# Kernel optimization log

Measured on AMD Instinct MI355X. Metric: run time of the kernel, lower is better.

## Reference

```python
import jax, jax.numpy as jnp
import numpy as np

N_NODES = 100000
N_EDGES = 1200000
IN_DIM, HID_DIM, OUT_DIM = 64, 64, 32


def setup_inputs() -> dict:
    key = jax.random.key(0)
    k1, k2, k3, k4, k5, k6 = jax.random.split(key, 6)
    x = jax.random.normal(k1, (N_NODES, IN_DIM), dtype=jnp.float32)
    edge_index = jax.random.randint(k2, (2, N_EDGES), 0, N_NODES, dtype=jnp.int64)
    # Glorot-style init for GCN linear weights
    W1 = jax.random.normal(k3, (IN_DIM, HID_DIM), dtype=jnp.float32) / np.sqrt(IN_DIM)
    b1 = jnp.zeros((HID_DIM,), dtype=jnp.float32)
    W2 = jax.random.normal(k4, (HID_DIM, OUT_DIM), dtype=jnp.float32) / np.sqrt(HID_DIM)
    b2 = jnp.zeros((OUT_DIM,), dtype=jnp.float32)
    return {"x": x, "edge_index": edge_index, "W1": W1, "b1": b1, "W2": W2, "b2": b2}


def _gcn_conv(x, W, b, src, dst, norm, n_nodes):
    # linear transform first (PyG GCNConv): [N, out]
    h = x @ W
    # gather messages along edges (incl. self-loops), scale by sym norm
    msg = h[src] * norm[:, None]            # [E+N, out]
    out = jax.ops.segment_sum(msg, dst, num_segments=n_nodes)
    return out + b


def reference(x, edge_index, W1, b1, W2, b2):
    n_nodes = x.shape[0]
    # add self-loops (PyG GCNConv default)
    loop = jnp.arange(n_nodes, dtype=edge_index.dtype)
    src = jnp.concatenate([edge_index[0], loop])
    dst = jnp.concatenate([edge_index[1], loop])
    # symmetric normalization: deg^{-1/2}[src] * deg^{-1/2}[dst]
    deg = jax.ops.segment_sum(jnp.ones_like(dst, dtype=x.dtype), dst, num_segments=n_nodes)
    deg_isqrt = jax.lax.rsqrt(deg)          # deg >= 1 due to self-loops
    norm = deg_isqrt[src] * deg_isqrt[dst]
    h = _gcn_conv(x, W1, b1, src, dst, norm, n_nodes)
    h = jax.nn.relu(h)
    out = _gcn_conv(h, W2, b2, src, dst, norm, n_nodes)
    return out
```

## Files before the change

### kernel.cpp

```cpp
#include <hip/hip_runtime.h>
#include <hip/hip_fp16.h>
#include <type_traits>

#define NBUCK 512
#define CH    2048

typedef _Float16 half8 __attribute__((ext_vector_type(8)));
typedef float floatx4 __attribute__((ext_vector_type(4)));

__device__ inline void unpack8(const float4& raw, float* f) {
    const __half2* p = (const __half2*)&raw;
#pragma unroll
    for (int i = 0; i < 4; ++i) {
        float2 t = __half22float2(p[i]);
        f[2 * i] = t.x;
        f[2 * i + 1] = t.y;
    }
}


__device__ inline void gemm64_f32_body(const float* __restrict__ X, const float* __restrict__ W,
                                       __half* __restrict__ H, int M, int ntiles, int vblk,
                                       int GB) {
    constexpr int NC = 4;
    const int lane = threadIdx.x & 63;
    const int wid  = threadIdx.x >> 6;
    const int q    = lane >> 4;
    const int m    = lane & 15;

    half8 bfrag[2][NC];
#pragma unroll
    for (int s = 0; s < 2; ++s)
#pragma unroll
        for (int c = 0; c < NC; ++c)
#pragma unroll
            for (int j = 0; j < 8; ++j)
                bfrag[s][c][j] = (_Float16)W[(s * 32 + q * 8 + j) * 64 + c * 16 + m];

    for (int tile = vblk * 4 + wid; tile < ntiles; tile += GB * 4) {
        int rowBase = tile * 16;
        int rowA = rowBase + m;
        if (rowA > M - 1) rowA = M - 1;

        half8 afrag[2];
        const float4* Xr = (const float4*)(X + (size_t)rowA * 64);
#pragma unroll
        for (int s = 0; s < 2; ++s) {
            float4 v0 = Xr[s * 8 + q * 2 + 0];
            float4 v1 = Xr[s * 8 + q * 2 + 1];
            afrag[s][0] = (_Float16)v0.x;
            afrag[s][1] = (_Float16)v0.y;
            afrag[s][2] = (_Float16)v0.z;
            afrag[s][3] = (_Float16)v0.w;
            afrag[s][4] = (_Float16)v1.x;
            afrag[s][5] = (_Float16)v1.y;
            afrag[s][6] = (_Float16)v1.z;
            afrag[s][7] = (_Float16)v1.w;
        }

        floatx4 acc[NC];
#pragma unroll
        for (int c = 0; c < NC; ++c) acc[c] = (floatx4){0.f, 0.f, 0.f, 0.f};
#pragma unroll
        for (int s = 0; s < 2; ++s)
#pragma unroll
            for (int c = 0; c < NC; ++c)
                acc[c] = __builtin_amdgcn_mfma_f32_16x16x32_f16(afrag[s], bfrag[s][c], acc[c],
                                                                0, 0, 0);

#pragma unroll
        for (int r = 0; r < 4; ++r) {
            int row = rowBase + q * 4 + r;
            if (row < M) {
#pragma unroll
                for (int c = 0; c < NC; ++c)
                    H[(size_t)row * 64 + c * 16 + m] = __float2half(acc[c][r]);
            }
        }
    }
}


__global__ __launch_bounds__(256) void hist_gemm1_kernel(
    const int* __restrict__ dst, int* __restrict__ blockHist,
    const float* __restrict__ X, const float* __restrict__ W1, __half* __restrict__ H,
    int M, int ntiles, int E, int R, int HB, int GB) {
    int blk = blockIdx.x;
    if (blk < HB) {
        __shared__ int h[NBUCK];
        int tid = threadIdx.x;
        for (int i = tid; i < NBUCK; i += 256) h[i] = 0;
        __syncthreads();
        int start = blk * CH;
        int count = E - start;
        if (count > CH) count = CH;
        for (int i = tid; i < count; i += 256) atomicAdd(&h[dst[start + i] / R], 1);
        __syncthreads();
        for (int i = tid; i < NBUCK; i += 256) blockHist[(size_t)blk * NBUCK + i] = h[i];
    } else {
        gemm64_f32_body(X, W1, H, M, ntiles, blk - HB, GB);
    }
}


__global__ __launch_bounds__(NBUCK) void scan_bases_kernel(const int* __restrict__ blockHist,
                                                           int* __restrict__ baseTbl,
                                                           int* __restrict__ bucketStart, int HB) {
    __shared__ int lds[NBUCK];
    int b = threadIdx.x;
    int running = 0;
    int k = 0;
    for (; k + 8 <= HB; k += 8) {
        int v[8];
#pragma unroll
        for (int u = 0; u < 8; ++u) v[u] = blockHist[(size_t)(k + u) * NBUCK + b];
#pragma unroll
        for (int u = 0; u < 8; ++u) {
            baseTbl[(size_t)(k + u) * NBUCK + b] = running;
            running += v[u];
        }
    }
    for (; k < HB; ++k) {
        int v = blockHist[(size_t)k * NBUCK + b];
        baseTbl[(size_t)k * NBUCK + b] = running;
        running += v;
    }
    lds[b] = running;
    __syncthreads();
    for (int off = 1; off < NBUCK; off <<= 1) {
        int x = (b >= off) ? lds[b - off] : 0;
        __syncthreads();
        lds[b] += x;
        __syncthreads();
    }
    bucketStart[b] = lds[b] - running;
    if (b == NBUCK - 1) bucketStart[NBUCK] = lds[b];
}


__global__ __launch_bounds__(256) void scatter_kernel(
    const int* __restrict__ src, const int* __restrict__ dst, const int* __restrict__ baseTbl,
    const int* __restrict__ bucketStart, unsigned long long* __restrict__ pairs, int E, int R) {
    __shared__ int lcur[NBUCK];
    int blk = blockIdx.x, tid = threadIdx.x;
    for (int i = tid; i < NBUCK; i += 256)
        lcur[i] = bucketStart[i] + baseTbl[(size_t)blk * NBUCK + i];
    __syncthreads();
    int start = blk * CH;
    int count = E - start;
    if (count > CH) count = CH;
    for (int i = tid; i < count; i += 256) {
        int d = dst[start + i];
        int s = src[start + i];
        int b = d / R;
        int r = atomicAdd(&lcur[b], 1);
        pairs[r] = ((unsigned long long)(unsigned)s << 32) | (unsigned)d;
    }
}


__global__ __launch_bounds__(256) void bucket_csr_kernel(
    const unsigned long long* __restrict__ pairs, const int* __restrict__ bucketStart,
    int* __restrict__ counts, int* __restrict__ offs, float* __restrict__ dinv,
    int* __restrict__ ssrc, int N, int R) {
    __shared__ unsigned long long stage[3072];
    __shared__ int h[256];
    __shared__ int loffs[256];
    __shared__ int cur[256];
    int b = blockIdx.x, tid = threadIdx.x;
    int nodeBase = b * R;
    int beg = bucketStart[b], end = bucketStart[b + 1];
    int len = end - beg;
    int sl = len < 3072 ? len : 3072;
    for (int i = tid; i < sl; i += 256) stage[i] = pairs[beg + i];
    h[tid] = 0;
    __syncthreads();
    for (int i = tid; i < len; i += 256) {
        unsigned long long p = (i < 3072) ? stage[i] : pairs[beg + i];
        atomicAdd(&h[(int)(p & 0xffffffffull) - nodeBase], 1);
    }
    __syncthreads();
    int v = h[tid];
    loffs[tid] = v;
    __syncthreads();
    for (int off = 1; off < 256; off <<= 1) {
        int x = (tid >= off) ? loffs[tid - off] : 0;
        __syncthreads();
        loffs[tid] += x;
        __syncthreads();
    }
    int excl = loffs[tid] - v;
    cur[tid] = excl;
    int node = nodeBase + tid;
    if (tid < R && node < N) {
        counts[node] = v;
        offs[node] = beg + excl;
        dinv[node] = rsqrtf((float)v + 1.0f);
    }
    __syncthreads();
    for (int i = tid; i < len; i += 256) {
        unsigned long long p = (i < 3072) ? stage[i] : pairs[beg + i];
        int d = (int)(p & 0xffffffffull) - nodeBase;
        int s = (int)(p >> 32);
        int r = atomicAdd(&cur[d], 1);
        ssrc[beg + r] = s;
    }
}


__global__ __launch_bounds__(256) void gemm2_mfma_kernel(const __half* __restrict__ X,
                                                         const float* __restrict__ W,
                                                         __half* __restrict__ H, int M,
                                                         int ntiles) {
    constexpr int NC = 2;
    const int lane = threadIdx.x & 63;
    const int wid  = threadIdx.x >> 6;
    const int q    = lane >> 4;
    const int m    = lane & 15;

    half8 bfrag[2][NC];
#pragma unroll
    for (int s = 0; s < 2; ++s)
#pragma unroll
        for (int c = 0; c < NC; ++c)
#pragma unroll
            for (int j = 0; j < 8; ++j)
                bfrag[s][c][j] = (_Float16)W[(s * 32 + q * 8 + j) * 32 + c * 16 + m];

    for (int tile = blockIdx.x * 4 + wid; tile < ntiles; tile += gridDim.x * 4) {
        int rowBase = tile * 16;
        int rowA = rowBase + m;
        if (rowA > M - 1) rowA = M - 1;

        const half8* Xr = (const half8*)(X + (size_t)rowA * 64);
        half8 afrag[2];
#pragma unroll
        for (int s = 0; s < 2; ++s) afrag[s] = Xr[s * 4 + q];

        floatx4 acc[NC];
#pragma unroll
        for (int c = 0; c < NC; ++c) acc[c] = (floatx4){0.f, 0.f, 0.f, 0.f};
#pragma unroll
        for (int s = 0; s < 2; ++s)
#pragma unroll
            for (int c = 0; c < NC; ++c)
                acc[c] = __builtin_amdgcn_mfma_f32_16x16x32_f16(afrag[s], bfrag[s][c], acc[c],
                                                                0, 0, 0);

#pragma unroll
        for (int r = 0; r < 4; ++r) {
            int row = rowBase + q * 4 + r;
            if (row < M) {
#pragma unroll
                for (int c = 0; c < NC; ++c)
                    H[(size_t)row * 32 + c * 16 + m] = __float2half(acc[c][r]);
            }
        }
    }
}


__global__ __launch_bounds__(256) void agg64_kernel(
    const float4* __restrict__ hrow4, const int* __restrict__ ssrc,
    const int* __restrict__ offs, const int* __restrict__ counts,
    const float* __restrict__ dinv, const float* __restrict__ b1,
    float4* __restrict__ out4, int N) {
    int tid  = threadIdx.x;
    int lane = tid & 63;
    int l    = tid & 7;
    int gb   = lane & 56;
    int node = blockIdx.x * 32 + (tid >> 3);
    if (node >= N) return;
    int beg = offs[node], cnt = counts[node];
    float a[8];
#pragma unroll
    for (int j = 0; j < 8; ++j) a[j] = 0.f;
    for (int base = 0; base < cnt; base += 8) {
        int p = base + l;
        int idx = 0;
        float dv = 0.0f;
        if (p < cnt) {
            idx = ssrc[beg + p];
            dv  = dinv[idx];
        }
#pragma unroll
        for (int j = 0; j < 8; ++j) {
            int   s  = __shfl(idx, gb | j, 64);
            float nv = __shfl(dv, gb | j, 64);
            float4 raw = hrow4[(size_t)s * 8 + l];
            float f[8];
            unpack8(raw, f);
#pragma unroll
            for (int d = 0; d < 8; ++d) a[d] = fmaf(f[d], nv, a[d]);
        }
    }
    float dd = dinv[node];
    float4 sraw = hrow4[(size_t)node * 8 + l];
    float sf[8];
    unpack8(sraw, sf);
    __half2 pk[4];
#pragma unroll
    for (int i = 0; i < 4; ++i) {
        float rx = fmaxf(dd * (a[2 * i] + sf[2 * i] * dd) + b1[8 * l + 2 * i], 0.0f);
        float ry = fmaxf(dd * (a[2 * i + 1] + sf[2 * i + 1] * dd) + b1[8 * l + 2 * i + 1], 0.0f);
        pk[i] = __floats2half2_rn(rx, ry);
    }
    out4[(size_t)node * 8 + l] = *(const float4*)pk;
}


__global__ __launch_bounds__(256) void agg32_kernel(
    const float4* __restrict__ hrow4, const int* __restrict__ ssrc,
    const int* __restrict__ offs, const int* __restrict__ counts,
    const float* __restrict__ dinv, const float* __restrict__ b2,
    float4* __restrict__ out4, int N) {
    int tid  = threadIdx.x;
    int lane = tid & 63;
    int l    = tid & 3;
    int gb   = lane & 60;
    int node = blockIdx.x * 64 + (tid >> 2);
    if (node >= N) return;
    int beg = offs[node], cnt = counts[node];
    float a[8];
#pragma unroll
    for (int j = 0; j < 8; ++j) a[j] = 0.f;
    for (int base = 0; base < cnt; base += 4) {
        int p = base + l;
        int idx = 0;
        float dv = 0.0f;
        if (p < cnt) {
            idx = ssrc[beg + p];
            dv  = dinv[idx];
        }
#pragma unroll
        for (int j = 0; j < 4; ++j) {
            int   s  = __shfl(idx, gb | j, 64);
            float nv = __shfl(dv, gb | j, 64);
            float4 raw = hrow4[(size_t)s * 4 + l];
            float f[8];
            unpack8(raw, f);
#pragma unroll
            for (int d = 0; d < 8; ++d) a[d] = fmaf(f[d], nv, a[d]);
        }
    }
    float dd = dinv[node];
    float4 sraw = hrow4[(size_t)node * 4 + l];
    float sf[8];
    unpack8(sraw, sf);
    float r[8];
#pragma unroll
    for (int j = 0; j < 8; ++j)
        r[j] = dd * (a[j] + sf[j] * dd) + b2[8 * l + j];
    out4[(size_t)node * 8 + 2 * l + 0] = make_float4(r[0], r[1], r[2], r[3]);
    out4[(size_t)node * 8 + 2 * l + 1] = make_float4(r[4], r[5], r[6], r[7]);
}


extern "C" void kernel_launch(void* const* d_in, const int* in_sizes, int n_in,
                              void* d_out, int out_size, void* d_ws, size_t ws_size,
                              hipStream_t stream) {
    const float* x  = (const float*)d_in[0];
    const int*   ei = (const int*)d_in[1];
    const float* W1 = (const float*)d_in[2];
    const float* b1 = (const float*)d_in[3];
    const float* W2 = (const float*)d_in[4];
    const float* b2 = (const float*)d_in[5];
    float* out = (float*)d_out;

    const int N = in_sizes[0] / 64;
    const int E = in_sizes[1] / 2;
    const int* src = ei;
    const int* dst = ei + E;

    const int Npad = (N + 1023) & ~1023;
    const int R    = (N + NBUCK - 1) / NBUCK;
    const int HB   = (E + CH - 1) / CH;
    const int GB   = 782;

    unsigned long long* pairs = (unsigned long long*)d_ws;
    int*   ssrc        = (int*)(pairs + E);
    int*   counts      = ssrc + E;
    int*   offs        = counts + Npad;
    float* dinv        = (float*)(offs + Npad);
    int*   bucketStart = (int*)(dinv + Npad);
    int*   blockHist   = bucketStart + NBUCK + 2;
    int*   baseTbl     = blockHist + (size_t)HB * NBUCK;
    size_t hoff = (size_t)(baseTbl + (size_t)HB * NBUCK - (int*)d_ws);
    hoff = (hoff + 3) & ~(size_t)3;
    __half* h    = (__half*)((int*)d_ws + hoff);
    __half* out1 = h + (size_t)N * 64;
    __half* h2   = h;

    const int ntiles = (N + 15) / 16;

    hist_gemm1_kernel<<<HB + GB, 256, 0, stream>>>(dst, blockHist, x, W1, h, N, ntiles,
                                                   E, R, HB, GB);
    scan_bases_kernel<<<1, NBUCK, 0, stream>>>(blockHist, baseTbl, bucketStart, HB);
    scatter_kernel<<<HB, 256, 0, stream>>>(src, dst, baseTbl, bucketStart, pairs, E, R);
    bucket_csr_kernel<<<NBUCK, 256, 0, stream>>>(pairs, bucketStart, counts, offs, dinv, ssrc,
                                                 N, R);
    agg64_kernel<<<(N + 31) / 32, 256, 0, stream>>>((const float4*)h, ssrc, offs, counts, dinv,
                                                    b1, (float4*)out1, N);
    gemm2_mfma_kernel<<<782, 256, 0, stream>>>(out1, W2, h2, N, ntiles);
    agg32_kernel<<<(N + 63) / 64, 256, 0, stream>>>((const float4*)h2, ssrc, offs, counts, dinv,
                                                    b2, (float4*)out, N);
}
```

Before: 227.3 us.

## Parallelize bucket base scan across blocks and double histogram chunk size

Replaces the single-block serial scan over all histogram blocks with a per-bucket parallel scan kernel (one block per bucket, two chunks per thread), followed by a small scan over bucket totals. The base table is stored transposed so each bucket's column is contiguous. The chunk size per histogram/scatter block is doubled, which halves the number of chunks so a 256-thread scan covers them all. The cost is an extra kernel launch, strided reads when the scatter kernel loads its bases, and the per-bucket scan only covering up to 512 chunks.

```diff
diff --git a/kernel.cpp b/kernel.cpp
--- a/kernel.cpp
+++ b/kernel.cpp
@@ -3,7 +3,7 @@
 #include <type_traits>
 
 #define NBUCK 512
-#define CH    2048
+#define CH    4096
 
 typedef _Float16 half8 __attribute__((ext_vector_type(8)));
 typedef float floatx4 __attribute__((ext_vector_type(4)));
@@ -103,29 +103,38 @@
 }
 
 
-__global__ __launch_bounds__(NBUCK) void scan_bases_kernel(const int* __restrict__ blockHist,
-                                                           int* __restrict__ baseTbl,
-                                                           int* __restrict__ bucketStart, int HB) {
+__global__ __launch_bounds__(256) void scan_cols_kernel(const int* __restrict__ blockHist,
+                                                        int* __restrict__ baseTblT,
+                                                        int* __restrict__ totals,
+                                                        int HB, int HBpad) {
+    __shared__ int lds[256];
+    int b = blockIdx.x;
+    int t = threadIdx.x;
+    int k0 = 2 * t, k1 = 2 * t + 1;
+    int v0 = (k0 < HB) ? blockHist[(size_t)k0 * NBUCK + b] : 0;
+    int v1 = (k1 < HB) ? blockHist[(size_t)k1 * NBUCK + b] : 0;
+    int s = v0 + v1;
+    lds[t] = s;
+    __syncthreads();
+    for (int off = 1; off < 256; off <<= 1) {
+        int x = (t >= off) ? lds[t - off] : 0;
+        __syncthreads();
+        lds[t] += x;
+        __syncthreads();
+    }
+    int excl = lds[t] - s;
+    if (k0 < HB) baseTblT[(size_t)b * HBpad + k0] = excl;
+    if (k1 < HB) baseTblT[(size_t)b * HBpad + k1] = excl + v0;
+    if (t == 255) totals[b] = lds[255];
+}
+
+
+__global__ __launch_bounds__(NBUCK) void scan_totals_kernel(const int* __restrict__ totals,
+                                                            int* __restrict__ bucketStart) {
     __shared__ int lds[NBUCK];
     int b = threadIdx.x;
-    int running = 0;
-    int k = 0;
-    for (; k + 8 <= HB; k += 8) {
-        int v[8];
-#pragma unroll
-        for (int u = 0; u < 8; ++u) v[u] = blockHist[(size_t)(k + u) * NBUCK + b];
-#pragma unroll
-        for (int u = 0; u < 8; ++u) {
-            baseTbl[(size_t)(k + u) * NBUCK + b] = running;
-            running += v[u];
-        }
-    }
-    for (; k < HB; ++k) {
-        int v = blockHist[(size_t)k * NBUCK + b];
-        baseTbl[(size_t)k * NBUCK + b] = running;
-        running += v;
-    }
-    lds[b] = running;
+    int v = totals[b];
+    lds[b] = v;
     __syncthreads();
     for (int off = 1; off < NBUCK; off <<= 1) {
         int x = (b >= off) ? lds[b - off] : 0;
@@ -133,18 +142,19 @@
         lds[b] += x;
         __syncthreads();
     }
-    bucketStart[b] = lds[b] - running;
+    bucketStart[b] = lds[b] - v;
     if (b == NBUCK - 1) bucketStart[NBUCK] = lds[b];
 }
 
 
 __global__ __launch_bounds__(256) void scatter_kernel(
-    const int* __restrict__ src, const int* __restrict__ dst, const int* __restrict__ baseTbl,
-    const int* __restrict__ bucketStart, unsigned long long* __restrict__ pairs, int E, int R) {
+    const int* __restrict__ src, const int* __restrict__ dst, const int* __restrict__ baseTblT,
+    const int* __restrict__ bucketStart, unsigned long long* __restrict__ pairs, int E, int R,
+    int HBpad) {
     __shared__ int lcur[NBUCK];
     int blk = blockIdx.x, tid = threadIdx.x;
     for (int i = tid; i < NBUCK; i += 256)
-        lcur[i] = bucketStart[i] + baseTbl[(size_t)blk * NBUCK + i];
+        lcur[i] = bucketStart[i] + baseTblT[(size_t)i * HBpad + blk];
     __syncthreads();
     int start = blk * CH;
     int count = E - start;
@@ -372,10 +382,11 @@
     const int* src = ei;
     const int* dst = ei + E;
 
-    const int Npad = (N + 1023) & ~1023;
-    const int R    = (N + NBUCK - 1) / NBUCK;
-    const int HB   = (E + CH - 1) / CH;
-    const int GB   = 782;
+    const int Npad  = (N + 1023) & ~1023;
+    const int R     = (N + NBUCK - 1) / NBUCK;
+    const int HB    = (E + CH - 1) / CH;
+    const int HBpad = (HB + 15) & ~15;
+    const int GB    = 782;
 
     unsigned long long* pairs = (unsigned long long*)d_ws;
     int*   ssrc        = (int*)(pairs + E);
@@ -383,9 +394,10 @@
     int*   offs        = counts + Npad;
     float* dinv        = (float*)(offs + Npad);
     int*   bucketStart = (int*)(dinv + Npad);
-    int*   blockHist   = bucketStart + NBUCK + 2;
-    int*   baseTbl     = blockHist + (size_t)HB * NBUCK;
-    size_t hoff = (size_t)(baseTbl + (size_t)HB * NBUCK - (int*)d_ws);
+    int*   totals      = bucketStart + NBUCK + 1;
+    int*   blockHist   = totals + NBUCK + 1;
+    int*   baseTblT    = blockHist + (size_t)HB * NBUCK;
+    size_t hoff = (size_t)(baseTblT + (size_t)NBUCK * HBpad - (int*)d_ws);
     hoff = (hoff + 3) & ~(size_t)3;
     __half* h    = (__half*)((int*)d_ws + hoff);
     __half* out1 = h + (size_t)N * 64;
@@ -395,8 +407,9 @@
 
     hist_gemm1_kernel<<<HB + GB, 256, 0, stream>>>(dst, blockHist, x, W1, h, N, ntiles,
                                                    E, R, HB, GB);
-    scan_bases_kernel<<<1, NBUCK, 0, stream>>>(blockHist, baseTbl, bucketStart, HB);
-    scatter_kernel<<<HB, 256, 0, stream>>>(src, dst, baseTbl, bucketStart, pairs, E, R);
+    scan_cols_kernel<<<NBUCK, 256, 0, stream>>>(blockHist, baseTblT, totals, HB, HBpad);
+    scan_totals_kernel<<<1, NBUCK, 0, stream>>>(totals, bucketStart);
+    scatter_kernel<<<HB, 256, 0, stream>>>(src, dst, baseTblT, bucketStart, pairs, E, R, HBpad);
     bucket_csr_kernel<<<NBUCK, 256, 0, stream>>>(pairs, bucketStart, counts, offs, dinv, ssrc,
                                                  N, R);
     agg64_kernel<<<(N + 31) / 32, 256, 0, stream>>>((const float4*)h, ssrc, offs, counts, dinv,
```

New measurement: 196.4 us. 1.16x faster.

## Fuse GCN pipeline into one cooperative persistent kernel with atomic bucket cursors

Applied to the files above, without the earlier changes.

Replaces the seven-kernel sequence with one cooperative persistent kernel that runs every phase and separates them with grid-wide syncs. A separate-kernel path remains as a fallback if the cooperative launch fails. The global scan over block histograms is dropped: each block claims its bucket ranges with atomicAdd on per-bucket cursors, and buckets sit at fixed capacity-strided slots (CAP=4096). The aim is to remove launch gaps and the serial single-block scan kernel. In exchange, buckets overflow if one receives more than 4096 edges, edge order inside a bucket becomes nondeterministic, and the persistent grid at 2 blocks per CU may lower occupancy for the aggregation phases.

```diff
diff --git a/kernel.cpp b/kernel.cpp
--- a/kernel.cpp
+++ b/kernel.cpp
@@ -1,12 +1,38 @@
 #include <hip/hip_runtime.h>
 #include <hip/hip_fp16.h>
-#include <type_traits>
+#include <hip/hip_cooperative_groups.h>
+
+namespace cg = cooperative_groups;
 
 #define NBUCK 512
-#define CH    2048
+#define CH    4096
+#define CAP   4096
+#define VTOT  1024
 
 typedef _Float16 half8 __attribute__((ext_vector_type(8)));
 typedef float floatx4 __attribute__((ext_vector_type(4)));
+
+struct Params {
+    const int* src;
+    const int* dst;
+    const float* x;
+    const float* W1;
+    const float* b1;
+    const float* W2;
+    const float* b2;
+    float* out;
+    int* baseTbl;
+    int* cursor;
+    unsigned long long* pairs;
+    int* ssrc;
+    int* counts;
+    int* offs;
+    float* dinv;
+    __half* h;
+    __half* out1;
+    __half* h2;
+    int N, E, R, HB, ntiles;
+};
 
 __device__ inline void unpack8(const float4& raw, float* f) {
     const __half2* p = (const __half2*)&raw;
@@ -18,21 +44,18 @@
     }
 }
 
-
-__device__ inline void gemm64_f32_body(const float* __restrict__ X, const float* __restrict__ W,
-                                       __half* __restrict__ H, int M, int ntiles, int vblk,
-                                       int GB) {
-    constexpr int NC = 4;
+__device__ void gemm1_body(const float* __restrict__ X, const float* __restrict__ W,
+                           __half* __restrict__ H, int M, int ntiles, int vblk, int GB) {
     const int lane = threadIdx.x & 63;
     const int wid  = threadIdx.x >> 6;
     const int q    = lane >> 4;
     const int m    = lane & 15;
 
-    half8 bfrag[2][NC];
+    half8 bfrag[2][4];
 #pragma unroll
     for (int s = 0; s < 2; ++s)
 #pragma unroll
-        for (int c = 0; c < NC; ++c)
+        for (int c = 0; c < 4; ++c)
 #pragma unroll
             for (int j = 0; j < 8; ++j)
                 bfrag[s][c][j] = (_Float16)W[(s * 32 + q * 8 + j) * 64 + c * 16 + m];
@@ -41,247 +64,186 @@
         int rowBase = tile * 16;
         int rowA = rowBase + m;
         if (rowA > M - 1) rowA = M - 1;
-
+        const float4* Xr = (const float4*)(X + (size_t)rowA * 64);
         half8 afrag[2];
-        const float4* Xr = (const float4*)(X + (size_t)rowA * 64);
 #pragma unroll
         for (int s = 0; s < 2; ++s) {
             float4 v0 = Xr[s * 8 + q * 2 + 0];
             float4 v1 = Xr[s * 8 + q * 2 + 1];
-            afrag[s][0] = (_Float16)v0.x;
-            afrag[s][1] = (_Float16)v0.y;
-            afrag[s][2] = (_Float16)v0.z;
-            afrag[s][3] = (_Float16)v0.w;
-            afrag[s][4] = (_Float16)v1.x;
-            afrag[s][5] = (_Float16)v1.y;
-            afrag[s][6] = (_Float16)v1.z;
-            afrag[s][7] = (_Float16)v1.w;
-        }
-
-        floatx4 acc[NC];
-#pragma unroll
-        for (int c = 0; c < NC; ++c) acc[c] = (floatx4){0.f, 0.f, 0.f, 0.f};
+            afrag[s][0] = (_Float16)v0.x; afrag[s][1] = (_Float16)v0.y;
+            afrag[s][2] = (_Float16)v0.z; afrag[s][3] = (_Float16)v0.w;
+            afrag[s][4] = (_Float16)v1.x; afrag[s][5] = (_Float16)v1.y;
+            afrag[s][6] = (_Float16)v1.z; afrag[s][7] = (_Float16)v1.w;
+        }
+        floatx4 acc[4];
+#pragma unroll
+        for (int c = 0; c < 4; ++c) acc[c] = (floatx4){0.f, 0.f, 0.f, 0.f};
 #pragma unroll
         for (int s = 0; s < 2; ++s)
 #pragma unroll
-            for (int c = 0; c < NC; ++c)
+            for (int c = 0; c < 4; ++c)
                 acc[c] = __builtin_amdgcn_mfma_f32_16x16x32_f16(afrag[s], bfrag[s][c], acc[c],
                                                                 0, 0, 0);
-
 #pragma unroll
         for (int r = 0; r < 4; ++r) {
             int row = rowBase + q * 4 + r;
             if (row < M) {
 #pragma unroll
-                for (int c = 0; c < NC; ++c)
+                for (int c = 0; c < 4; ++c)
                     H[(size_t)row * 64 + c * 16 + m] = __float2half(acc[c][r]);
             }
         }
     }
 }
 
-
-__global__ __launch_bounds__(256) void hist_gemm1_kernel(
-    const int* __restrict__ dst, int* __restrict__ blockHist,
-    const float* __restrict__ X, const float* __restrict__ W1, __half* __restrict__ H,
-    int M, int ntiles, int E, int R, int HB, int GB) {
-    int blk = blockIdx.x;
-    if (blk < HB) {
-        __shared__ int h[NBUCK];
-        int tid = threadIdx.x;
-        for (int i = tid; i < NBUCK; i += 256) h[i] = 0;
-        __syncthreads();
-        int start = blk * CH;
-        int count = E - start;
-        if (count > CH) count = CH;
-        for (int i = tid; i < count; i += 256) atomicAdd(&h[dst[start + i] / R], 1);
-        __syncthreads();
-        for (int i = tid; i < NBUCK; i += 256) blockHist[(size_t)blk * NBUCK + i] = h[i];
-    } else {
-        gemm64_f32_body(X, W1, H, M, ntiles, blk - HB, GB);
-    }
-}
-
-
-__global__ __launch_bounds__(NBUCK) void scan_bases_kernel(const int* __restrict__ blockHist,
-                                                           int* __restrict__ baseTbl,
-                                                           int* __restrict__ bucketStart, int HB) {
-    __shared__ int lds[NBUCK];
-    int b = threadIdx.x;
-    int running = 0;
-    int k = 0;
-    for (; k + 8 <= HB; k += 8) {
-        int v[8];
-#pragma unroll
-        for (int u = 0; u < 8; ++u) v[u] = blockHist[(size_t)(k + u) * NBUCK + b];
-#pragma unroll
-        for (int u = 0; u < 8; ++u) {
-            baseTbl[(size_t)(k + u) * NBUCK + b] = running;
-            running += v[u];
-        }
-    }
-    for (; k < HB; ++k) {
-        int v = blockHist[(size_t)k * NBUCK + b];
-        baseTbl[(size_t)k * NBUCK + b] = running;
-        running += v;
-    }
-    lds[b] = running;
-    __syncthreads();
-    for (int off = 1; off < NBUCK; off <<= 1) {
-        int x = (b >= off) ? lds[b - off] : 0;
-        __syncthreads();
-        lds[b] += x;
-        __syncthreads();
-    }
-    bucketStart[b] = lds[b] - running;
-    if (b == NBUCK - 1) bucketStart[NBUCK] = lds[b];
-}
-
-
-__global__ __launch_bounds__(256) void scatter_kernel(
-    const int* __restrict__ src, const int* __restrict__ dst, const int* __restrict__ baseTbl,
-    const int* __restrict__ bucketStart, unsigned long long* __restrict__ pairs, int E, int R) {
-    __shared__ int lcur[NBUCK];
-    int blk = blockIdx.x, tid = threadIdx.x;
-    for (int i = tid; i < NBUCK; i += 256)
-        lcur[i] = bucketStart[i] + baseTbl[(size_t)blk * NBUCK + i];
-    __syncthreads();
-    int start = blk * CH;
-    int count = E - start;
-    if (count > CH) count = CH;
-    for (int i = tid; i < count; i += 256) {
-        int d = dst[start + i];
-        int s = src[start + i];
-        int b = d / R;
-        int r = atomicAdd(&lcur[b], 1);
-        pairs[r] = ((unsigned long long)(unsigned)s << 32) | (unsigned)d;
-    }
-}
-
-
-__global__ __launch_bounds__(256) void bucket_csr_kernel(
-    const unsigned long long* __restrict__ pairs, const int* __restrict__ bucketStart,
-    int* __restrict__ counts, int* __restrict__ offs, float* __restrict__ dinv,
-    int* __restrict__ ssrc, int N, int R) {
-    __shared__ unsigned long long stage[3072];
-    __shared__ int h[256];
-    __shared__ int loffs[256];
-    __shared__ int cur[256];
-    int b = blockIdx.x, tid = threadIdx.x;
-    int nodeBase = b * R;
-    int beg = bucketStart[b], end = bucketStart[b + 1];
-    int len = end - beg;
-    int sl = len < 3072 ? len : 3072;
-    for (int i = tid; i < sl; i += 256) stage[i] = pairs[beg + i];
-    h[tid] = 0;
-    __syncthreads();
-    for (int i = tid; i < len; i += 256) {
-        unsigned long long p = (i < 3072) ? stage[i] : pairs[beg + i];
-        atomicAdd(&h[(int)(p & 0xffffffffull) - nodeBase], 1);
-    }
-    __syncthreads();
-    int v = h[tid];
-    loffs[tid] = v;
-    __syncthreads();
-    for (int off = 1; off < 256; off <<= 1) {
-        int x = (tid >= off) ? loffs[tid - off] : 0;
-        __syncthreads();
-        loffs[tid] += x;
-        __syncthreads();
-    }
-    int excl = loffs[tid] - v;
-    cur[tid] = excl;
-    int node = nodeBase + tid;
-    if (tid < R && node < N) {
-        counts[node] = v;
-        offs[node] = beg + excl;
-        dinv[node] = rsqrtf((float)v + 1.0f);
-    }
-    __syncthreads();
-    for (int i = tid; i < len; i += 256) {
-        unsigned long long p = (i < 3072) ? stage[i] : pairs[beg + i];
-        int d = (int)(p & 0xffffffffull) - nodeBase;
-        int s = (int)(p >> 32);
-        int r = atomicAdd(&cur[d], 1);
-        ssrc[beg + r] = s;
-    }
-}
-
-
-__global__ __launch_bounds__(256) void gemm2_mfma_kernel(const __half* __restrict__ X,
-                                                         const float* __restrict__ W,
-                                                         __half* __restrict__ H, int M,
-                                                         int ntiles) {
-    constexpr int NC = 2;
+__device__ void gemm2_body(const __half* __restrict__ X, const float* __restrict__ W,
+                           __half* __restrict__ H, int M, int ntiles, int vblk, int GB) {
     const int lane = threadIdx.x & 63;
     const int wid  = threadIdx.x >> 6;
     const int q    = lane >> 4;
     const int m    = lane & 15;
 
-    half8 bfrag[2][NC];
+    half8 bfrag[2][2];
 #pragma unroll
     for (int s = 0; s < 2; ++s)
 #pragma unroll
-        for (int c = 0; c < NC; ++c)
+        for (int c = 0; c < 2; ++c)
 #pragma unroll
             for (int j = 0; j < 8; ++j)
                 bfrag[s][c][j] = (_Float16)W[(s * 32 + q * 8 + j) * 32 + c * 16 + m];
 
-    for (int tile = blockIdx.x * 4 + wid; tile < ntiles; tile += gridDim.x * 4) {
+    for (int tile = vblk * 4 + wid; tile < ntiles; tile += GB * 4) {
         int rowBase = tile * 16;
         int rowA = rowBase + m;
         if (rowA > M - 1) rowA = M - 1;
-
         const half8* Xr = (const half8*)(X + (size_t)rowA * 64);
         half8 afrag[2];
 #pragma unroll
         for (int s = 0; s < 2; ++s) afrag[s] = Xr[s * 4 + q];
-
-        floatx4 acc[NC];
-#pragma unroll
-        for (int c = 0; c < NC; ++c) acc[c] = (floatx4){0.f, 0.f, 0.f, 0.f};
+        floatx4 acc[2];
+#pragma unroll
+        for (int c = 0; c < 2; ++c) acc[c] = (floatx4){0.f, 0.f, 0.f, 0.f};
 #pragma unroll
         for (int s = 0; s < 2; ++s)
 #pragma unroll
-            for (int c = 0; c < NC; ++c)
+            for (int c = 0; c < 2; ++c)
                 acc[c] = __builtin_amdgcn_mfma_f32_16x16x32_f16(afrag[s], bfrag[s][c], acc[c],
                                                                 0, 0, 0);
-
 #pragma unroll
         for (int r = 0; r < 4; ++r) {
             int row = rowBase + q * 4 + r;
             if (row < M) {
 #pragma unroll
-                for (int c = 0; c < NC; ++c)
+                for (int c = 0; c < 2; ++c)
                     H[(size_t)row * 32 + c * 16 + m] = __float2half(acc[c][r]);
             }
         }
     }
 }
 
-
-__global__ __launch_bounds__(256) void agg64_kernel(
-    const float4* __restrict__ hrow4, const int* __restrict__ ssrc,
-    const int* __restrict__ offs, const int* __restrict__ counts,
-    const float* __restrict__ dinv, const float* __restrict__ b1,
-    float4* __restrict__ out4, int N) {
-    int tid  = threadIdx.x;
+__device__ void phase_hist(const Params& p, int vb) {
+    __shared__ int h[NBUCK];
+    int tid = threadIdx.x;
+    __syncthreads();
+    for (int i = tid; i < NBUCK; i += 256) h[i] = 0;
+    __syncthreads();
+    int start = vb * CH;
+    int count = p.E - start;
+    if (count > CH) count = CH;
+    for (int i = tid; i < count; i += 256) atomicAdd(&h[p.dst[start + i] / p.R], 1);
+    __syncthreads();
+    for (int i = tid; i < NBUCK; i += 256) {
+        int c = h[i];
+        int base = c ? atomicAdd(&p.cursor[i], c) : 0;
+        p.baseTbl[(size_t)vb * NBUCK + i] = base;
+    }
+}
+
+__device__ void phase_scatter(const Params& p, int vb) {
+    __shared__ int lcur[NBUCK];
+    int tid = threadIdx.x;
+    __syncthreads();
+    for (int i = tid; i < NBUCK; i += 256)
+        lcur[i] = i * CAP + p.baseTbl[(size_t)vb * NBUCK + i];
+    __syncthreads();
+    int start = vb * CH;
+    int count = p.E - start;
+    if (count > CH) count = CH;
+    for (int i = tid; i < count; i += 256) {
+        int d = p.dst[start + i];
+        int s = p.src[start + i];
+        int b = d / p.R;
+        int r = atomicAdd(&lcur[b], 1);
+        p.pairs[r] = ((unsigned long long)(unsigned)s << 32) | (unsigned)d;
+    }
+}
+
+__device__ void phase_csr(const Params& p, int b) {
+    __shared__ unsigned long long stage[2048];
+    __shared__ int h[256];
+    __shared__ int loffs[256];
+    __shared__ int cur[256];
+    int tid = threadIdx.x;
+    __syncthreads();
+    int nodeBase = b * p.R;
+    int beg = b * CAP;
+    int len = p.cursor[b];
+    int sl = len < 2048 ? len : 2048;
+    for (int i = tid; i < sl; i += 256) stage[i] = p.pairs[beg + i];
+    h[tid] = 0;
+    __syncthreads();
+    for (int i = tid; i < len; i += 256) {
+        unsigned long long pr = (i < 2048) ? stage[i] : p.pairs[beg + i];
+        atomicAdd(&h[(int)(pr & 0xffffffffull) - nodeBase], 1);
+    }
+    __syncthreads();
+    int v = h[tid];
+    loffs[tid] = v;
+    __syncthreads();
+    for (int off = 1; off < 256; off <<= 1) {
+        int xv = (tid >= off) ? loffs[tid - off] : 0;
+        __syncthreads();
+        loffs[tid] += xv;
+        __syncthreads();
+    }
+    int excl = loffs[tid] - v;
+    cur[tid] = excl;
+    int node = nodeBase + tid;
+    if (tid < p.R && node < p.N) {
+        p.counts[node] = v;
+        p.offs[node] = beg + excl;
+        p.dinv[node] = rsqrtf((float)v + 1.0f);
+    }
+    __syncthreads();
+    for (int i = tid; i < len; i += 256) {
+        unsigned long long pr = (i < 2048) ? stage[i] : p.pairs[beg + i];
+        int d = (int)(pr & 0xffffffffull) - nodeBase;
+        int s = (int)(pr >> 32);
+        int r = atomicAdd(&cur[d], 1);
+        p.ssrc[beg + r] = s;
+    }
+}
+
+__device__ void phase_agg64(const Params& p, int vb) {
+    const float4* hrow4 = (const float4*)p.h;
+    float4* out4 = (float4*)p.out1;
+    int tid = threadIdx.x;
     int lane = tid & 63;
-    int l    = tid & 7;
-    int gb   = lane & 56;
-    int node = blockIdx.x * 32 + (tid >> 3);
-    if (node >= N) return;
-    int beg = offs[node], cnt = counts[node];
+    int l  = tid & 7;
+    int gb = lane & 56;
+    int node = vb * 32 + (tid >> 3);
+    if (node >= p.N) return;
+    int beg = p.offs[node], cnt = p.counts[node];
     float a[8];
 #pragma unroll
     for (int j = 0; j < 8; ++j) a[j] = 0.f;
     for (int base = 0; base < cnt; base += 8) {
-        int p = base + l;
+        int pos = base + l;
         int idx = 0;
         float dv = 0.0f;
-        if (p < cnt) {
-            idx = ssrc[beg + p];
-            dv  = dinv[idx];
+        if (pos < cnt) {
+            idx = p.ssrc[beg + pos];
+            dv  = p.dinv[idx];
         }
 #pragma unroll
         for (int j = 0; j < 8; ++j) {
@@ -294,43 +256,40 @@
             for (int d = 0; d < 8; ++d) a[d] = fmaf(f[d], nv, a[d]);
         }
     }
-    float dd = dinv[node];
+    float dd = p.dinv[node];
     float4 sraw = hrow4[(size_t)node * 8 + l];
     float sf[8];
     unpack8(sraw, sf);
     __half2 pk[4];
 #pragma unroll
     for (int i = 0; i < 4; ++i) {
-        float rx = fmaxf(dd * (a[2 * i] + sf[2 * i] * dd) + b1[8 * l + 2 * i], 0.0f);
-        float ry = fmaxf(dd * (a[2 * i + 1] + sf[2 * i + 1] * dd) + b1[8 * l + 2 * i + 1], 0.0f);
+        float rx = fmaxf(dd * (a[2 * i] + sf[2 * i] * dd) + p.b1[8 * l + 2 * i], 0.0f);
+        float ry = fmaxf(dd * (a[2 * i + 1] + sf[2 * i + 1] * dd) + p.b1[8 * l + 2 * i + 1], 0.0f);
         pk[i] = __floats2half2_rn(rx, ry);
     }
     out4[(size_t)node * 8 + l] = *(const float4*)pk;
 }
 
-
-__global__ __launch_bounds__(256) void agg32_kernel(
-    const float4* __restrict__ hrow4, const int* __restrict__ ssrc,
-    const int* __restrict__ offs, const int* __restrict__ counts,
-    const float* __restrict__ dinv, const float* __restrict__ b2,
-    float4* __restrict__ out4, int N) {
-    int tid  = threadIdx.x;
+__device__ void phase_agg32(const Params& p, int vb) {
+    const float4* hrow4 = (const float4*)p.h2;
+    float4* out4 = (float4*)p.out;
+    int tid = threadIdx.x;
     int lane = tid & 63;
-    int l    = tid & 3;
-    int gb   = lane & 60;
-    int node = blockIdx.x * 64 + (tid >> 2);
-    if (node >= N) return;
-    int beg = offs[node], cnt = counts[node];
+    int l  = tid & 3;
+    int gb = lane & 60;
+    int node = vb * 64 + (tid >> 2);
+    if (node >= p.N) return;
+    int beg = p.offs[node], cnt = p.counts[node];
     float a[8];
 #pragma unroll
     for (int j = 0; j < 8; ++j) a[j] = 0.f;
     for (int base = 0; base < cnt; base += 4) {
-        int p = base + l;
+        int pos = base + l;
         int idx = 0;
         float dv = 0.0f;
-        if (p < cnt) {
-            idx = ssrc[beg + p];
-            dv  = dinv[idx];
+        if (pos < cnt) {
+            idx = p.ssrc[beg + pos];
+            dv  = p.dinv[idx];
         }
 #pragma unroll
         for (int j = 0; j < 4; ++j) {
@@ -343,17 +302,50 @@
             for (int d = 0; d < 8; ++d) a[d] = fmaf(f[d], nv, a[d]);
         }
     }
-    float dd = dinv[node];
+    float dd = p.dinv[node];
     float4 sraw = hrow4[(size_t)node * 4 + l];
     float sf[8];
     unpack8(sraw, sf);
     float r[8];
 #pragma unroll
     for (int j = 0; j < 8; ++j)
-        r[j] = dd * (a[j] + sf[j] * dd) + b2[8 * l + j];
+        r[j] = dd * (a[j] + sf[j] * dd) + p.b2[8 * l + j];
     out4[(size_t)node * 8 + 2 * l + 0] = make_float4(r[0], r[1], r[2], r[3]);
     out4[(size_t)node * 8 + 2 * l + 1] = make_float4(r[4], r[5], r[6], r[7]);
 }
+
+__global__ __launch_bounds__(256, 2) void mega_kernel(Params p) {
+    cg::grid_group grid = cg::this_grid();
+    for (int vb = blockIdx.x; vb < VTOT; vb += gridDim.x) {
+        if (vb < p.HB) phase_hist(p, vb);
+        else gemm1_body(p.x, p.W1, p.h, p.N, p.ntiles, vb - p.HB, VTOT - p.HB);
+    }
+    grid.sync();
+    for (int vb = blockIdx.x; vb < p.HB; vb += gridDim.x) phase_scatter(p, vb);
+    grid.sync();
+    for (int b = blockIdx.x; b < NBUCK; b += gridDim.x) phase_csr(p, b);
+    grid.sync();
+    int nvb64 = (p.N + 31) >> 5;
+    for (int vb = blockIdx.x; vb < nvb64; vb += gridDim.x) phase_agg64(p, vb);
+    grid.sync();
+    gemm2_body(p.out1, p.W2, p.h2, p.N, p.ntiles, blockIdx.x, gridDim.x);
+    grid.sync();
+    int nvb32 = (p.N + 63) >> 6;
+    for (int vb = blockIdx.x; vb < nvb32; vb += gridDim.x) phase_agg32(p, vb);
+}
+
+__global__ __launch_bounds__(256) void k_phaseA(Params p) {
+    int vb = blockIdx.x;
+    if (vb < p.HB) phase_hist(p, vb);
+    else gemm1_body(p.x, p.W1, p.h, p.N, p.ntiles, vb - p.HB, VTOT - p.HB);
+}
+__global__ __launch_bounds__(256) void k_scatter(Params p) { phase_scatter(p, blockIdx.x); }
+__global__ __launch_bounds__(256) void k_csr(Params p) { phase_csr(p, blockIdx.x); }
+__global__ __launch_bounds__(256) void k_agg64(Params p) { phase_agg64(p, blockIdx.x); }
+__global__ __launch_bounds__(256) void k_gemm2(Params p) {
+    gemm2_body(p.out1, p.W2, p.h2, p.N, p.ntiles, blockIdx.x, gridDim.x);
+}
+__global__ __launch_bounds__(256) void k_agg32(Params p) { phase_agg32(p, blockIdx.x); }
 
 
 extern "C" void kernel_launch(void* const* d_in, const int* in_sizes, int n_in,
@@ -365,43 +357,56 @@
     const float* b1 = (const float*)d_in[3];
     const float* W2 = (const float*)d_in[4];
     const float* b2 = (const float*)d_in[5];
-    float* out = (float*)d_out;
 
     const int N = in_sizes[0] / 64;
     const int E = in_sizes[1] / 2;
-    const int* src = ei;
-    const int* dst = ei + E;
 
     const int Npad = (N + 1023) & ~1023;
     const int R    = (N + NBUCK - 1) / NBUCK;
     const int HB   = (E + CH - 1) / CH;
-    const int GB   = 782;
-
-    unsigned long long* pairs = (unsigned long long*)d_ws;
-    int*   ssrc        = (int*)(pairs + E);
-    int*   counts      = ssrc + E;
-    int*   offs        = counts + Npad;
-    float* dinv        = (float*)(offs + Npad);
-    int*   bucketStart = (int*)(dinv + Npad);
-    int*   blockHist   = bucketStart + NBUCK + 2;
-    int*   baseTbl     = blockHist + (size_t)HB * NBUCK;
-    size_t hoff = (size_t)(baseTbl + (size_t)HB * NBUCK - (int*)d_ws);
-    hoff = (hoff + 3) & ~(size_t)3;
-    __half* h    = (__half*)((int*)d_ws + hoff);
-    __half* out1 = h + (size_t)N * 64;
+
+    char* w = (char*)d_ws;
+    unsigned long long* pairs = (unsigned long long*)w;  w += (size_t)NBUCK * CAP * 8;
+    int*   ssrc    = (int*)w;                            w += (size_t)NBUCK * CAP * 4;
+    int*   counts  = (int*)w;                            w += (size_t)Npad * 4;
+    int*   offs    = (int*)w;                            w += (size_t)Npad * 4;
+    float* dinv    = (float*)w;                          w += (size_t)Npad * 4;
+    int*   baseTbl = (int*)w;                            w += (size_t)HB * NBUCK * 4;
+    int*   cursor  = (int*)w;                            w += (size_t)(NBUCK + 4) * 4;
+    __half* h    = (__half*)w;                           w += (size_t)N * 64 * 2;
+    __half* out1 = (__half*)w;                           w += (size_t)N * 64 * 2;
     __half* h2   = h;
 
-    const int ntiles = (N + 15) / 16;
-
-    hist_gemm1_kernel<<<HB + GB, 256, 0, stream>>>(dst, blockHist, x, W1, h, N, ntiles,
-                                                   E, R, HB, GB);
-    scan_bases_kernel<<<1, NBUCK, 0, stream>>>(blockHist, baseTbl, bucketStart, HB);
-    scatter_kernel<<<HB, 256, 0, stream>>>(src, dst, baseTbl, bucketStart, pairs, E, R);
-    bucket_csr_kernel<<<NBUCK, 256, 0, stream>>>(pairs, bucketStart, counts, offs, dinv, ssrc,
-                                                 N, R);
-    agg64_kernel<<<(N + 31) / 32, 256, 0, stream>>>((const float4*)h, ssrc, offs, counts, dinv,
-                                                    b1, (float4*)out1, N);
-    gemm2_mfma_kernel<<<782, 256, 0, stream>>>(out1, W2, h2, N, ntiles);
-    agg32_kernel<<<(N + 63) / 64, 256, 0, stream>>>((const float4*)h2, ssrc, offs, counts, dinv,
-                                                    b2, (float4*)out, N);
-}
+    hipMemsetAsync(cursor, 0, NBUCK * sizeof(int), stream);
+
+    Params p;
+    p.src = ei;
+    p.dst = ei + E;
+    p.x = x; p.W1 = W1; p.b1 = b1; p.W2 = W2; p.b2 = b2;
+    p.out = (float*)d_out;
+    p.baseTbl = baseTbl; p.cursor = cursor;
+    p.pairs = pairs; p.ssrc = ssrc;
+    p.counts = counts; p.offs = offs; p.dinv = dinv;
+    p.h = h; p.out1 = out1; p.h2 = h2;
+    p.N = N; p.E = E; p.R = R; p.HB = HB;
+    p.ntiles = (N + 15) / 16;
+
+    int occ = 0;
+    hipOccupancyMaxActiveBlocksPerMultiprocessor(&occ, mega_kernel, 256, 0);
+    hipError_t err = hipErrorUnknown;
+    if (occ > 0) {
+        int grid = occ * 256;
+        if (grid > VTOT) grid = VTOT;
+        void* args[] = {&p};
+        err = hipLaunchCooperativeKernel((const void*)mega_kernel, dim3(grid), dim3(256),
+                                         args, 0, stream);
+    }
+    if (err != hipSuccess) {
+        k_phaseA<<<VTOT, 256, 0, stream>>>(p);
+        k_scatter<<<HB, 256, 0, stream>>>(p);
+        k_csr<<<NBUCK, 256, 0, stream>>>(p);
+        k_agg64<<<(N + 31) / 32, 256, 0, stream>>>(p);
+        k_gemm2<<<782, 256, 0, stream>>>(p);
+        k_agg32<<<(N + 63) / 64, 256, 0, stream>>>(p);
+    }
+}
```

Result: slower. 420.5 us (+85.0%).
